# Optimization experiments

Hardware: AMD Instinct MI355X
Metric: run time of the kernel (lower is better)

The kernel has to match this reference:

```python
import jax, jax.numpy as jnp
import numpy as np

NUM_PID = 5532
QUEUE_SIZE = 5000
DIM = 256
BATCH = 4096


def _l2norm(x, axis=-1, eps=1e-12):
    return x / jnp.maximum(jnp.linalg.norm(x, axis=axis, keepdims=True), eps)


def setup_inputs() -> dict:
    key = jax.random.key(0)
    k1, k2, k3, k4, k5 = jax.random.split(key, 5)
    inputs = _l2norm(jax.random.normal(k1, (BATCH, DIM), dtype=jnp.float32))
    # targets in [-1, NUM_PID): -1 marks unlabeled identities (go to the circular queue)
    targets = jax.random.randint(k2, (BATCH,), -1, NUM_PID)
    gt_flag = jax.random.bernoulli(k3, 0.5, (BATCH,))
    lut = _l2norm(jax.random.normal(k4, (NUM_PID, DIM), dtype=jnp.float32))
    queue = _l2norm(jax.random.normal(k5, (QUEUE_SIZE, DIM), dtype=jnp.float32))
    return {"inputs": inputs, "targets": targets, "gt_flag": gt_flag, "lut": lut, "queue": queue}


def reference(inputs, targets, gt_flag, lut, queue):
    # MatchFunction.forward (lut.dim()==2 path): similarity of features against
    # the labeled lookup table and the unlabeled circular queue.
    outputs_labeled = inputs @ lut.T            # [B, num_pid]
    outputs_unlabeled = inputs @ queue.T        # [B, Q]
    return jnp.concatenate([outputs_labeled, outputs_unlabeled], axis=1)
```

## Files before the change

kernel.cpp:

```cpp
#include <hip/hip_runtime.h>
#include <hip/hip_bf16.h>
#include <stdint.h>


#define M_DIM 4096
#define K_DIM 256
#define N_LUT 5532
#define N_Q   5000
#define N_DIM (N_LUT + N_Q)
#define BN    256
#define NT_N  42
#define N_PAD (NT_N * 256)
#define NSTRIP 6

typedef _Float16 f16x8 __attribute__((ext_vector_type(8)));
typedef float f32x4 __attribute__((ext_vector_type(4)));

__device__ __forceinline__ unsigned short f2h(float f) {
  union { _Float16 h; unsigned short u; } v;
  v.h = (_Float16)f;
  return v.u;
}

__global__ __launch_bounds__(256) void convert_kernel(
    const float* __restrict__ inp, const float* __restrict__ lut,
    const float* __restrict__ que, unsigned short* __restrict__ Abf,
    unsigned short* __restrict__ Bbf) {
  const int AV = M_DIM * K_DIM / 4;
  int i = blockIdx.x * 256 + threadIdx.x;
  float4 x;
  unsigned short* dst;
  if (i < AV) {
    x = ((const float4*)inp)[i];
    dst = Abf + i * 4;
  } else {
    int e = (i - AV) * 4;
    int row = e >> 8;
    int col = e & 255;
    if (row < N_LUT)
      x = *(const float4*)(lut + (size_t)row * K_DIM + col);
    else if (row < N_DIM)
      x = *(const float4*)(que + (size_t)(row - N_LUT) * K_DIM + col);
    else
      x = make_float4(0.f, 0.f, 0.f, 0.f);
    dst = Bbf + e;
  }
  ushort4 o;
  o.x = f2h(x.x); o.y = f2h(x.y); o.z = f2h(x.z); o.w = f2h(x.w);
  *(ushort4*)dst = o;
}

#define GLDS16(gsrc, ldst)                                                  \
  __builtin_amdgcn_global_load_lds(                                         \
      (__attribute__((address_space(1))) void*)(gsrc),                      \
      (__attribute__((address_space(3))) void*)(ldst), 16, 0, 0)

__global__ __launch_bounds__(512, 2) void gemm_kernel(
    const unsigned short* __restrict__ A, const unsigned short* __restrict__ B,
    float* __restrict__ C) {
  __shared__ __align__(16) unsigned short As[2][32 * 256];

  const int t = threadIdx.x;
  const int lane = t & 63;
  const int wave = t >> 6;

  const int bid = blockIdx.x;
  const int bn = bid % NT_N;
  const int s = bid / NT_N;
  const int bcol = bn * BN;
  const bool fullN = (bcol + BN <= N_DIM);
  const int csub = 21 + (s >= 4 ? 1 : 0);
  const int sub0 = 21 * s + (s >= 5 ? 1 : 0);
  const int row0 = sub0 * 32;

  const int lr = lane & 15;
  const int rsw = lane & 7;
  const int cq = lane >> 4;
  const int cc4 = cq * 4;

  f16x8 breg[2][8];
#pragma unroll
  for (int j = 0; j < 2; ++j) {
    const unsigned short* brow =
        B + (size_t)(bcol + wave * 32 + j * 16 + lr) * K_DIM + cq * 8;
#pragma unroll
    for (int ks = 0; ks < 8; ++ks)
      breg[j][ks] = *(const f16x8*)(brow + ks * 32);
  }

  const int srow = t >> 5;
  const int scs = (((t & 31) ^ (srow & 7)) * 8);
  const unsigned short* gaBase0 = A + (size_t)(row0 + srow) * K_DIM + scs;
  const int ldsRound = wave * 2 * 256;

#define STAGE_A(buf, sub)                                                    \
  do {                                                                       \
    _Pragma("unroll") for (int r = 0; r < 2; ++r)                            \
      GLDS16(gaBase0 + ((size_t)(sub) * 32 + r * 16) * K_DIM,                \
             As[buf] + r * 16 * 256 + ldsRound);                             \
  } while (0)

  STAGE_A(0, 0);
  __syncthreads();

  int cur = 0;
#pragma unroll 1
  for (int sub = 0; sub < csub; ++sub) {
    if (sub + 1 < csub)
      STAGE_A(cur ^ 1, sub + 1);
    __builtin_amdgcn_sched_barrier(0);

    f32x4 acc[2][2] = {};
#pragma unroll
    for (int ks = 0; ks < 8; ++ks) {
      const int ch = (ks * 4 + cq) ^ rsw;
      f16x8 a[2];
#pragma unroll
      for (int i = 0; i < 2; ++i)
        a[i] = *(const f16x8*)&As[cur][(i * 16 + lr) * 256 + ch * 8];
#pragma unroll
      for (int i = 0; i < 2; ++i)
#pragma unroll
        for (int j = 0; j < 2; ++j)
          acc[i][j] = __builtin_amdgcn_mfma_f32_16x16x32_f16(breg[j][ks], a[i],
                                                             acc[i][j], 0, 0, 0);
    }

#pragma unroll
    for (int i = 0; i < 2; ++i) {
      size_t rowBase = (size_t)(row0 + sub * 32 + i * 16 + lr) * N_DIM;
#pragma unroll
      for (int j = 0; j < 2; ++j) {
        int col = bcol + wave * 32 + j * 16 + cc4;
        if (col < N_DIM)
          *(f32x4*)&C[rowBase + col] = acc[i][j];
      }
    }

    if (sub + 1 < csub) {
      if (fullN)
        asm volatile("s_waitcnt vmcnt(4)" ::: "memory");
      else
        asm volatile("s_waitcnt vmcnt(0)" ::: "memory");
      asm volatile("s_barrier" ::: "memory");
    }
    cur ^= 1;
  }
#undef STAGE_A
}

extern "C" void kernel_launch(void* const* d_in, const int* in_sizes, int n_in,
                              void* d_out, int out_size, void* d_ws, size_t ws_size,
                              hipStream_t stream) {
  const float* inp = (const float*)d_in[0];
  const float* lut = (const float*)d_in[3];
  const float* que = (const float*)d_in[4];
  float* C = (float*)d_out;

  unsigned short* Abf = (unsigned short*)d_ws;
  unsigned short* Bbf = Abf + (size_t)M_DIM * K_DIM;

  const int conv_blocks = (M_DIM * K_DIM / 4 + N_PAD * K_DIM / 4) / 256;
  convert_kernel<<<conv_blocks, 256, 0, stream>>>(inp, lut, que, Abf, Bbf);

  gemm_kernel<<<NSTRIP * NT_N, 512, 0, stream>>>(Abf, Bbf, C);
}
```

Baseline: 48.38 us.

## Load A tiles directly from global into registers, dropping LDS staging and barriers

The GEMM kernel no longer stages A sub-tiles through double-buffered LDS via global_load_lds with barriers. Each wave now loads its A fragments straight from global memory into registers and unrolls the strip loop by two. Occupancy hints drop to one block per CU. This removes LDS traffic and block-wide synchronisation, but each of the eight waves now reads the same A rows redundantly from cache, and register pressure rises, which may hurt latency hiding.

After: 106.6 us. 120% more time.

```diff
diff --git a/kernel.cpp b/kernel.cpp
--- a/kernel.cpp
+++ b/kernel.cpp
@@ -50,16 +50,9 @@
   *(ushort4*)dst = o;
 }
 
-#define GLDS16(gsrc, ldst)                                                  \
-  __builtin_amdgcn_global_load_lds(                                         \
-      (__attribute__((address_space(1))) void*)(gsrc),                      \
-      (__attribute__((address_space(3))) void*)(ldst), 16, 0, 0)
-
-__global__ __launch_bounds__(512, 2) void gemm_kernel(
+__global__ __launch_bounds__(512, 1) void gemm_kernel(
     const unsigned short* __restrict__ A, const unsigned short* __restrict__ B,
     float* __restrict__ C) {
-  __shared__ __align__(16) unsigned short As[2][32 * 256];
-
   const int t = threadIdx.x;
   const int lane = t & 63;
   const int wave = t >> 6;
@@ -68,13 +61,11 @@
   const int bn = bid % NT_N;
   const int s = bid / NT_N;
   const int bcol = bn * BN;
-  const bool fullN = (bcol + BN <= N_DIM);
   const int csub = 21 + (s >= 4 ? 1 : 0);
   const int sub0 = 21 * s + (s >= 5 ? 1 : 0);
   const int row0 = sub0 * 32;
 
   const int lr = lane & 15;
-  const int rsw = lane & 7;
   const int cq = lane >> 4;
   const int cc4 = cq * 4;
 
@@ -88,43 +79,27 @@
       breg[j][ks] = *(const f16x8*)(brow + ks * 32);
   }
 
-  const int srow = t >> 5;
-  const int scs = (((t & 31) ^ (srow & 7)) * 8);
-  const unsigned short* gaBase0 = A + (size_t)(row0 + srow) * K_DIM + scs;
-  const int ldsRound = wave * 2 * 256;
+  const unsigned short* aBase = A + (size_t)(row0 + lr) * K_DIM + cq * 8;
 
-#define STAGE_A(buf, sub)                                                    \
-  do {                                                                       \
-    _Pragma("unroll") for (int r = 0; r < 2; ++r)                            \
-      GLDS16(gaBase0 + ((size_t)(sub) * 32 + r * 16) * K_DIM,                \
-             As[buf] + r * 16 * 256 + ldsRound);                             \
-  } while (0)
-
-  STAGE_A(0, 0);
-  __syncthreads();
-
-  int cur = 0;
-#pragma unroll 1
+#pragma unroll 2
   for (int sub = 0; sub < csub; ++sub) {
-    if (sub + 1 < csub)
-      STAGE_A(cur ^ 1, sub + 1);
-    __builtin_amdgcn_sched_barrier(0);
+    const unsigned short* ap = aBase + (size_t)sub * 32 * K_DIM;
+    f16x8 a[2][8];
+#pragma unroll
+    for (int i = 0; i < 2; ++i)
+#pragma unroll
+      for (int ks = 0; ks < 8; ++ks)
+        a[i][ks] = *(const f16x8*)(ap + i * 16 * K_DIM + ks * 32);
 
     f32x4 acc[2][2] = {};
 #pragma unroll
-    for (int ks = 0; ks < 8; ++ks) {
-      const int ch = (ks * 4 + cq) ^ rsw;
-      f16x8 a[2];
-#pragma unroll
-      for (int i = 0; i < 2; ++i)
-        a[i] = *(const f16x8*)&As[cur][(i * 16 + lr) * 256 + ch * 8];
+    for (int ks = 0; ks < 8; ++ks)
 #pragma unroll
       for (int i = 0; i < 2; ++i)
 #pragma unroll
         for (int j = 0; j < 2; ++j)
-          acc[i][j] = __builtin_amdgcn_mfma_f32_16x16x32_f16(breg[j][ks], a[i],
-                                                             acc[i][j], 0, 0, 0);
-    }
+          acc[i][j] = __builtin_amdgcn_mfma_f32_16x16x32_f16(
+              breg[j][ks], a[i][ks], acc[i][j], 0, 0, 0);
 
 #pragma unroll
     for (int i = 0; i < 2; ++i) {
@@ -136,17 +111,7 @@
           *(f32x4*)&C[rowBase + col] = acc[i][j];
       }
     }
-
-    if (sub + 1 < csub) {
-      if (fullN)
-        asm volatile("s_waitcnt vmcnt(4)" ::: "memory");
-      else
-        asm volatile("s_waitcnt vmcnt(0)" ::: "memory");
-      asm volatile("s_barrier" ::: "memory");
-    }
-    cur ^= 1;
   }
-#undef STAGE_A
 }
 
 extern "C" void kernel_launch(void* const* d_in, const int* in_sizes, int n_in,
```
